# Kernel optimization log

Measured on AMD Instinct MI355X. Metric: run time of the kernel, lower is better.

Reference implementation:

```python
import jax, jax.numpy as jnp
import numpy as np

T, H, E, F, K, FS = 2048, 2048, 64, 512, 8, 512


def setup_inputs() -> dict:
    key = jax.random.key(0)
    ks = jax.random.split(key, 6)
    s = 0.02
    return {
        "hidden_states": jax.random.normal(ks[0], (T, H), jnp.float32),
        # merged gate: E router logits + 1 shared-expert gate logit
        "W_gate": jax.random.normal(ks[1], (H, E + 1), jnp.float32) * s,
        # per-expert merged gate_up proj: [E, H, 2F]
        "W_gate_up": jax.random.normal(ks[2], (E, H, 2 * F), jnp.float32) * s,
        "W_down": jax.random.normal(ks[3], (E, F, H), jnp.float32) * s,
        # shared expert
        "Ws_gate_up": jax.random.normal(ks[4], (H, 2 * FS), jnp.float32) * s,
        "Ws_down": jax.random.normal(ks[5], (FS, H), jnp.float32) * s,
    }


def reference(hidden_states, W_gate, W_gate_up, W_down, Ws_gate_up, Ws_down):
    x = hidden_states  # [T, H]
    logits_all = x @ W_gate                      # [T, E+1]
    router_logits = logits_all[:, :E]
    shared_gate_logit = logits_all[:, E:]        # [T, 1]

    # FusedMoE routing: softmax -> top_k -> renormalize (norm_topk_prob=True)
    probs = jax.nn.softmax(router_logits.astype(jnp.float32), axis=-1)
    topk_w, topk_idx = jax.lax.top_k(probs, K)   # [T, K]
    topk_w = topk_w / jnp.sum(topk_w, axis=-1, keepdims=True)
    # dense combine weights [T, E] (zero for unselected experts)
    combine = jnp.zeros((T, E), probs.dtype).at[
        jnp.arange(T)[:, None], topk_idx].set(topk_w)

    # grouped expert GEMMs (dense reference: every expert sees all tokens,
    # combine-weights zero-out unrouted pairs)
    gu = jnp.einsum('th,ehf->etf', x, W_gate_up)   # [E, T, 2F]
    g, u = jnp.split(gu, 2, axis=-1)
    act = jax.nn.silu(g) * u                       # [E, T, F]
    # apply combine weight before down-proj to avoid [E, T, H] intermediate
    act = act * combine.T[:, :, None].astype(act.dtype)
    routed = jnp.einsum('etf,efh->th', act, W_down)  # [T, H]

    # shared expert (Qwen3NextMLP with sigmoid expert_gate)
    sgu = x @ Ws_gate_up                           # [T, 2FS]
    sg, su = jnp.split(sgu, 2, axis=-1)
    shared = (jax.nn.silu(sg) * su) @ Ws_down      # [T, H]
    shared = jax.nn.sigmoid(shared_gate_logit) * shared

    return shared + routed.astype(x.dtype)
```

## Files before the change

kernel.cpp:

```cpp
#include <hip/hip_runtime.h>
#include <hip/hip_bf16.h>
#include <math.h>

#define T_TOK 2048
#define H_DIM 2048
#define E_NUM 64
#define F_DIM 512
#define K_TOP 8
#define FS_DIM 512
#define NROWS (T_TOK * K_TOP)

typedef __attribute__((ext_vector_type(8))) short short8v;
typedef __attribute__((ext_vector_type(4))) float f32x4;

static __device__ __forceinline__ unsigned short f2bf(float f) {
    unsigned int u = __float_as_uint(f);
    u += 0x7fff + ((u >> 16) & 1);
    return (unsigned short)(u >> 16);
}

__global__ __launch_bounds__(256) void cvt_bf16_kernel(
    const float* __restrict__ in, unsigned short* __restrict__ out, int n8)
{
    int i = blockIdx.x * 256 + threadIdx.x;
    if (i < n8) {
        const float4* p = (const float4*)(in + (size_t)i * 8);
        float4 v0 = p[0], v1 = p[1];
        ushort4 a = make_ushort4(f2bf(v0.x), f2bf(v0.y), f2bf(v0.z), f2bf(v0.w));
        ushort4 b = make_ushort4(f2bf(v1.x), f2bf(v1.y), f2bf(v1.z), f2bf(v1.w));
        ushort4* q = (ushort4*)(out + (size_t)i * 8);
        q[0] = a; q[1] = b;
    }
}

__global__ __launch_bounds__(64) void router_kernel(
    const float* __restrict__ x, const float* __restrict__ Wg,
    int* __restrict__ topk_idx, float* __restrict__ topk_w,
    float* __restrict__ sgate, int* __restrict__ counts)
{
    const int t = blockIdx.x;
    const int lane = threadIdx.x;
    const float* xr = x + (size_t)t * H_DIM;

    float a0 = 0.f, a1 = 0.f, a2 = 0.f, a3 = 0.f;
    for (int h = 0; h < H_DIM; h += 4) {
        float4 xv = *(const float4*)&xr[h];
        a0 += xv.x * Wg[(h + 0) * 65 + lane];
        a1 += xv.y * Wg[(h + 1) * 65 + lane];
        a2 += xv.z * Wg[(h + 2) * 65 + lane];
        a3 += xv.w * Wg[(h + 3) * 65 + lane];
    }
    float logit = (a0 + a1) + (a2 + a3);

    float a64 = 0.f;
    for (int h = lane; h < H_DIM; h += 64) a64 += xr[h] * Wg[h * 65 + 64];
#pragma unroll
    for (int off = 32; off >= 1; off >>= 1) a64 += __shfl_xor(a64, off);

    float v = logit;
    float selv[K_TOP]; int seli[K_TOP];
#pragma unroll
    for (int k = 0; k < K_TOP; ++k) {
        float mv = v; int mi = lane;
#pragma unroll
        for (int off = 32; off >= 1; off >>= 1) {
            float ov = __shfl_xor(mv, off);
            int   oi = __shfl_xor(mi, off);
            if (ov > mv || (ov == mv && oi < mi)) { mv = ov; mi = oi; }
        }
        selv[k] = mv; seli[k] = mi;
        if (lane == mi) v = -INFINITY;
    }

    if (lane == 0) {
        float m = selv[0];
        float w[K_TOP]; float s = 0.f;
#pragma unroll
        for (int k = 0; k < K_TOP; ++k) { w[k] = __expf(selv[k] - m); s += w[k]; }
        float inv = 1.f / s;
#pragma unroll
        for (int k = 0; k < K_TOP; ++k) {
            topk_idx[t * K_TOP + k] = seli[k];
            topk_w[t * K_TOP + k] = w[k] * inv;
            atomicAdd(&counts[seli[k]], 1);
        }
        sgate[t] = 1.f / (1.f + __expf(-a64));
    }
}

__global__ __launch_bounds__(256) void bucket_kernel(
    const int* __restrict__ topk_idx, const float* __restrict__ topk_w,
    const int* __restrict__ counts, int* __restrict__ offsets,
    int* __restrict__ bucket_tok, float* __restrict__ bucket_w)
{
    const int e = blockIdx.x, thr = threadIdx.x;
    __shared__ int cnt[256];
    __shared__ int base_s;
    const int q0 = thr * 64;
    int c = 0;
    for (int q = 0; q < 64; ++q) c += (topk_idx[q0 + q] == e) ? 1 : 0;
    cnt[thr] = c;
    __syncthreads();
    if (thr == 0) {
        int off = 0;
        for (int i = 0; i < e; ++i) off += counts[i];
        offsets[e] = off;
        base_s = off;
        int run = 0;
        for (int i = 0; i < 256; ++i) { int tval = cnt[i]; cnt[i] = run; run += tval; }
    }
    __syncthreads();
    int pos = base_s + cnt[thr];
    for (int q = 0; q < 64; ++q) {
        int pp = q0 + q;
        if (topk_idx[pp] == e) {
            bucket_tok[pos] = pp >> 3;
            bucket_w[pos] = topk_w[pp];
            ++pos;
        }
    }
}

template<int FM, bool ROUTED>
__global__ __launch_bounds__(512, 4) void gu_mfma_kernel(
    const unsigned short* __restrict__ xb,
    const float* __restrict__ Wall,
    const int* __restrict__ counts, const int* __restrict__ offsets,
    const int* __restrict__ bucket_tok, const float* __restrict__ bucket_w,
    unsigned short* __restrict__ actout)
{
    constexpr int BM = FM * 64;
    __shared__ __align__(16) unsigned short Bs[64 * 64];
    __shared__ int   toksS[BM];
    __shared__ float twsS[BM];

    const int tid  = threadIdx.x;
    const int lane = tid & 63;
    const int wid  = tid >> 6;
    const int wm = wid >> 1, wn = wid & 1;
    const int lrow = lane & 15, lhi = lane >> 4;
    const int lr7  = lrow & 7;

    const int c0 = blockIdx.x * 32;
    int ne, base;
    const float* W;
    if (ROUTED) {
        int e = blockIdx.y;
        ne = counts[e]; base = offsets[e];
        W = Wall + (size_t)e * H_DIM * (2 * F_DIM);
    } else {
        ne = T_TOK; base = 0;
        W = Wall;
    }

    const int n4 = (tid & 15) * 4;
    const int kb = (tid >> 4) * 2;
    const int n5 = n4 & 31;
    const int wcol = ((n5 < 16) ? 0 : (F_DIM - 16)) + c0 + (n4 >> 5) * 16 + n5;

    const int m0_beg = ROUTED ? 0 : blockIdx.y * BM;
    const int m0_end = ROUTED ? ne : m0_beg + BM;

    for (int m0 = m0_beg; m0 < m0_end; m0 += BM) {
        __syncthreads();
        for (int i = tid; i < BM; i += 512) {
            if (ROUTED) {
                int idx = m0 + i; bool v = idx < ne;
                toksS[i] = v ? bucket_tok[base + idx] : bucket_tok[base];
                twsS[i]  = v ? bucket_w[base + idx] : 0.f;
            } else {
                toksS[i] = m0 + i; twsS[i] = 1.f;
            }
        }
        __syncthreads();

        const unsigned short* aptr[FM];
#pragma unroll
        for (int fm = 0; fm < FM; ++fm) {
            int r = wm * (FM * 16) + fm * 16 + lrow;
            aptr[fm] = xb + (size_t)toksS[r] * H_DIM;
        }

        f32x4 acc[FM][2];
#pragma unroll
        for (int i = 0; i < FM; ++i) {
            acc[i][0] = (f32x4){0.f, 0.f, 0.f, 0.f};
            acc[i][1] = (f32x4){0.f, 0.f, 0.f, 0.f};
        }

        float4 b0 = *(const float4*)&W[(size_t)kb * (2 * F_DIM) + wcol];
        float4 b1 = *(const float4*)&W[(size_t)(kb + 1) * (2 * F_DIM) + wcol];

        const int NT = H_DIM / 64;
        for (int kt = 0; kt < NT; ++kt) {
#pragma unroll
            for (int cc = 0; cc < 4; ++cc) {
                int n = n4 + cc;
                int idx = n * 64 + ((((kb >> 3) ^ (n & 7)) << 3)) + (kb & 7);
                ushort2 p = make_ushort2(f2bf(((const float*)&b0)[cc]),
                                         f2bf(((const float*)&b1)[cc]));
                *(ushort2*)&Bs[idx] = p;
            }
            __syncthreads();
            if (kt + 1 < NT) {
                const int k0n = (kt + 1) * 64;
                b0 = *(const float4*)&W[(size_t)(k0n + kb) * (2 * F_DIM) + wcol];
                b1 = *(const float4*)&W[(size_t)(k0n + kb + 1) * (2 * F_DIM) + wcol];
            }
            const int k0 = kt * 64;
#pragma unroll
            for (int ks = 0; ks < 2; ++ks) {
                const int kc = ks * 4 + lhi;
                short8v bg = *(const short8v*)&Bs[(wn * 32 + lrow) * 64 + ((kc ^ lr7) << 3)];
                short8v bu = *(const short8v*)&Bs[(wn * 32 + 16 + lrow) * 64 + ((kc ^ lr7) << 3)];
                const int koff = k0 + kc * 8;
#pragma unroll
                for (int fm = 0; fm < FM; ++fm) {
                    short8v af = *(const short8v*)(aptr[fm] + koff);
                    acc[fm][0] = __builtin_amdgcn_mfma_f32_16x16x32_bf16(af, bg, acc[fm][0], 0, 0, 0);
                    acc[fm][1] = __builtin_amdgcn_mfma_f32_16x16x32_bf16(af, bu, acc[fm][1], 0, 0, 0);
                }
            }
            __syncthreads();
        }

        const int acol = c0 + wn * 16 + lrow;
#pragma unroll
        for (int fm = 0; fm < FM; ++fm) {
#pragma unroll
            for (int i = 0; i < 4; ++i) {
                int ml = wm * (FM * 16) + fm * 16 + lhi * 4 + i;
                int idx = m0 + ml;
                if (!ROUTED || idx < ne) {
                    float gv = acc[fm][0][i], uv = acc[fm][1][i];
                    float s = gv / (1.f + __expf(-gv));
                    float val = s * uv * twsS[ml];
                    size_t orow = ROUTED ? (size_t)(base + idx) : (size_t)idx;
                    actout[orow * F_DIM + acol] = f2bf(val);
                }
            }
        }
    }
}

template<int FM, bool ROUTED>
__global__ __launch_bounds__(512, 4) void down_mfma_kernel(
    const unsigned short* __restrict__ actb,
    const float* __restrict__ Wall,
    const int* __restrict__ counts, const int* __restrict__ offsets,
    const int* __restrict__ bucket_tok, const float* __restrict__ sgate,
    float* __restrict__ out)
{
    constexpr int BM = FM * 64;
    __shared__ __align__(16) unsigned short Bs[64 * 64];
    __shared__ int   toksS[BM];
    __shared__ float sgS[BM];

    const int tid  = threadIdx.x;
    const int lane = tid & 63;
    const int wid  = tid >> 6;
    const int wm = wid >> 1, wn = wid & 1;
    const int lrow = lane & 15, lhi = lane >> 4;
    const int lr7  = lrow & 7;

    const int c0 = blockIdx.x * 64;
    int ne, base;
    const float* W;
    if (ROUTED) {
        int e = blockIdx.y;
        ne = counts[e]; base = offsets[e];
        W = Wall + (size_t)e * F_DIM * H_DIM;
    } else {
        ne = T_TOK; base = 0;
        W = Wall;
    }

    const int n4 = (tid & 15) * 4;
    const int kb = (tid >> 4) * 2;
    const int wcol = c0 + n4;

    const int m0_beg = ROUTED ? 0 : blockIdx.y * BM;
    const int m0_end = ROUTED ? ne : m0_beg + BM;

    for (int m0 = m0_beg; m0 < m0_end; m0 += BM) {
        __syncthreads();
        for (int i = tid; i < BM; i += 512) {
            if (ROUTED) {
                int idx = m0 + i;
                toksS[i] = (idx < ne) ? bucket_tok[base + idx] : 0;
            } else {
                sgS[i] = sgate[m0 + i];
            }
        }
        __syncthreads();

        const unsigned short* aptr[FM];
#pragma unroll
        for (int fm = 0; fm < FM; ++fm) {
            int r = wm * (FM * 16) + fm * 16 + lrow;
            int grow = ROUTED ? min(base + m0 + r, NROWS - 1) : (m0 + r);
            aptr[fm] = actb + (size_t)grow * F_DIM;
        }

        f32x4 acc[FM][2];
#pragma unroll
        for (int i = 0; i < FM; ++i) {
            acc[i][0] = (f32x4){0.f, 0.f, 0.f, 0.f};
            acc[i][1] = (f32x4){0.f, 0.f, 0.f, 0.f};
        }

        float4 b0 = *(const float4*)&W[(size_t)kb * H_DIM + wcol];
        float4 b1 = *(const float4*)&W[(size_t)(kb + 1) * H_DIM + wcol];

        const int NT = F_DIM / 64;
        for (int kt = 0; kt < NT; ++kt) {
#pragma unroll
            for (int cc = 0; cc < 4; ++cc) {
                int n = n4 + cc;
                int idx = n * 64 + ((((kb >> 3) ^ (n & 7)) << 3)) + (kb & 7);
                ushort2 p = make_ushort2(f2bf(((const float*)&b0)[cc]),
                                         f2bf(((const float*)&b1)[cc]));
                *(ushort2*)&Bs[idx] = p;
            }
            __syncthreads();
            if (kt + 1 < NT) {
                const int k0n = (kt + 1) * 64;
                b0 = *(const float4*)&W[(size_t)(k0n + kb) * H_DIM + wcol];
                b1 = *(const float4*)&W[(size_t)(k0n + kb + 1) * H_DIM + wcol];
            }
            const int k0 = kt * 64;
#pragma unroll
            for (int ks = 0; ks < 2; ++ks) {
                const int kc = ks * 4 + lhi;
                short8v bf0 = *(const short8v*)&Bs[(wn * 32 + lrow) * 64 + ((kc ^ lr7) << 3)];
                short8v bf1 = *(const short8v*)&Bs[(wn * 32 + 16 + lrow) * 64 + ((kc ^ lr7) << 3)];
                const int koff = k0 + kc * 8;
#pragma unroll
                for (int fm = 0; fm < FM; ++fm) {
                    short8v af = *(const short8v*)(aptr[fm] + koff);
                    acc[fm][0] = __builtin_amdgcn_mfma_f32_16x16x32_bf16(af, bf0, acc[fm][0], 0, 0, 0);
                    acc[fm][1] = __builtin_amdgcn_mfma_f32_16x16x32_bf16(af, bf1, acc[fm][1], 0, 0, 0);
                }
            }
            __syncthreads();
        }

#pragma unroll
        for (int fm = 0; fm < FM; ++fm) {
#pragma unroll
            for (int fn = 0; fn < 2; ++fn) {
                int col = c0 + wn * 32 + fn * 16 + lrow;
#pragma unroll
                for (int i = 0; i < 4; ++i) {
                    int ml = wm * (FM * 16) + fm * 16 + lhi * 4 + i;
                    int idx = m0 + ml;
                    if (ROUTED) {
                        if (idx < ne)
                            atomicAdd(&out[(size_t)toksS[ml] * H_DIM + col], acc[fm][fn][i]);
                    } else {
                        out[(size_t)idx * H_DIM + col] = sgS[ml] * acc[fm][fn][i];
                    }
                }
            }
        }
    }
}

extern "C" void kernel_launch(void* const* d_in, const int* in_sizes, int n_in,
                              void* d_out, int out_size, void* d_ws, size_t ws_size,
                              hipStream_t stream) {
    const float* x    = (const float*)d_in[0];
    const float* Wg   = (const float*)d_in[1];
    const float* Wgu  = (const float*)d_in[2];
    const float* Wd   = (const float*)d_in[3];
    const float* Wsgu = (const float*)d_in[4];
    const float* Wsd  = (const float*)d_in[5];
    float* out = (float*)d_out;

    char* p = (char*)d_ws;
    auto alloc = [&](size_t bytes) {
        char* r = p;
        p += (bytes + 255) & ~(size_t)255;
        return r;
    };
    int*   topk_idx   = (int*)  alloc((size_t)T_TOK * K_TOP * sizeof(int));
    float* topk_w     = (float*)alloc((size_t)T_TOK * K_TOP * sizeof(float));
    float* sgate      = (float*)alloc((size_t)T_TOK * sizeof(float));
    int*   counts     = (int*)  alloc((size_t)E_NUM * sizeof(int));
    int*   offsets    = (int*)  alloc((size_t)E_NUM * sizeof(int));
    int*   bucket_tok = (int*)  alloc((size_t)NROWS * sizeof(int));
    float* bucket_w   = (float*)alloc((size_t)NROWS * sizeof(float));
    unsigned short* xb    = (unsigned short*)alloc((size_t)T_TOK * H_DIM * sizeof(short));
    unsigned short* act_r = (unsigned short*)alloc((size_t)NROWS * F_DIM * sizeof(short));
    unsigned short* act_s = (unsigned short*)alloc((size_t)T_TOK * FS_DIM * sizeof(short));

    hipMemsetAsync(counts, 0, E_NUM * sizeof(int), stream);
    cvt_bf16_kernel<<<(T_TOK * H_DIM / 8 + 255) / 256, 256, 0, stream>>>(x, xb, T_TOK * H_DIM / 8);
    router_kernel<<<T_TOK, 64, 0, stream>>>(x, Wg, topk_idx, topk_w, sgate, counts);
    bucket_kernel<<<E_NUM, 256, 0, stream>>>(topk_idx, topk_w, counts, offsets, bucket_tok, bucket_w);

    gu_mfma_kernel<5, true><<<dim3(16, E_NUM), 512, 0, stream>>>(
        xb, Wgu, counts, offsets, bucket_tok, bucket_w, act_r);
    gu_mfma_kernel<2, false><<<dim3(16, T_TOK / 128), 512, 0, stream>>>(
        xb, Wsgu, counts, offsets, bucket_tok, bucket_w, act_s);

    down_mfma_kernel<2, false><<<dim3(32, T_TOK / 128), 512, 0, stream>>>(
        act_s, Wsd, counts, offsets, bucket_tok, sgate, out);
    down_mfma_kernel<5, true><<<dim3(32, E_NUM), 512, 0, stream>>>(
        act_r, Wd, counts, offsets, bucket_tok, sgate, out);
}
```

Measured before the change: 866.0 us.

## Double-buffer weight tiles in LDS, prefetch A fragments, remap routed blocks across XCDs

Both MFMA GEMM kernels now keep two LDS buffers for the bf16 weight tile, so the next tile is converted and stored while the current one is consumed. That cuts one barrier per k-step. A-operand fragments for the whole k-tile are loaded into registers before the MFMAs. The XOR swizzle is replaced with a padded row stride of 72. Routed launches become 1D grids whose block index is permuted so that blocks of the same expert land on the same XCD, aiming at better L2 reuse of expert weights. The cost is doubled LDS and more registers per thread, which may reduce occupancy under launch_bounds(512,4).

```diff
diff --git a/kernel.cpp b/kernel.cpp
--- a/kernel.cpp
+++ b/kernel.cpp
@@ -130,7 +130,8 @@
     unsigned short* __restrict__ actout)
 {
     constexpr int BM = FM * 64;
-    __shared__ __align__(16) unsigned short Bs[64 * 64];
+    constexpr int BST = 72;
+    __shared__ __align__(16) unsigned short Bs[2][64 * BST];
     __shared__ int   toksS[BM];
     __shared__ float twsS[BM];
 
@@ -139,19 +140,20 @@
     const int wid  = tid >> 6;
     const int wm = wid >> 1, wn = wid & 1;
     const int lrow = lane & 15, lhi = lane >> 4;
-    const int lr7  = lrow & 7;
-
-    const int c0 = blockIdx.x * 32;
-    int ne, base;
+
+    int cblk, ne, base;
     const float* W;
     if (ROUTED) {
-        int e = blockIdx.y;
+        int nw = (blockIdx.x & 7) * ((int)gridDim.x >> 3) + (blockIdx.x >> 3);
+        int e = nw >> 4; cblk = nw & 15;
         ne = counts[e]; base = offsets[e];
         W = Wall + (size_t)e * H_DIM * (2 * F_DIM);
     } else {
+        cblk = blockIdx.x;
         ne = T_TOK; base = 0;
         W = Wall;
     }
+    const int c0 = cblk * 32;
 
     const int n4 = (tid & 15) * 4;
     const int kb = (tid >> 4) * 2;
@@ -188,37 +190,55 @@
             acc[i][1] = (f32x4){0.f, 0.f, 0.f, 0.f};
         }
 
-        float4 b0 = *(const float4*)&W[(size_t)kb * (2 * F_DIM) + wcol];
-        float4 b1 = *(const float4*)&W[(size_t)(kb + 1) * (2 * F_DIM) + wcol];
+        {
+            float4 b0 = *(const float4*)&W[(size_t)kb * (2 * F_DIM) + wcol];
+            float4 b1 = *(const float4*)&W[(size_t)(kb + 1) * (2 * F_DIM) + wcol];
+#pragma unroll
+            for (int cc = 0; cc < 4; ++cc) {
+                ushort2 pk = make_ushort2(f2bf(((const float*)&b0)[cc]),
+                                          f2bf(((const float*)&b1)[cc]));
+                *(ushort2*)&Bs[0][(n4 + cc) * BST + kb] = pk;
+            }
+        }
+        __syncthreads();
 
         const int NT = H_DIM / 64;
         for (int kt = 0; kt < NT; ++kt) {
-#pragma unroll
-            for (int cc = 0; cc < 4; ++cc) {
-                int n = n4 + cc;
-                int idx = n * 64 + ((((kb >> 3) ^ (n & 7)) << 3)) + (kb & 7);
-                ushort2 p = make_ushort2(f2bf(((const float*)&b0)[cc]),
-                                         f2bf(((const float*)&b1)[cc]));
-                *(ushort2*)&Bs[idx] = p;
-            }
-            __syncthreads();
+            const int k0 = kt * 64;
+            const unsigned short* curB = Bs[kt & 1];
+            unsigned short* nxtB = Bs[(kt & 1) ^ 1];
+
+            short8v a[2][FM];
+#pragma unroll
+            for (int ks = 0; ks < 2; ++ks)
+#pragma unroll
+                for (int fm = 0; fm < FM; ++fm)
+                    a[ks][fm] = *(const short8v*)(aptr[fm] + k0 + (ks * 4 + lhi) * 8);
+
+            float4 b0, b1;
             if (kt + 1 < NT) {
-                const int k0n = (kt + 1) * 64;
-                b0 = *(const float4*)&W[(size_t)(k0n + kb) * (2 * F_DIM) + wcol];
-                b1 = *(const float4*)&W[(size_t)(k0n + kb + 1) * (2 * F_DIM) + wcol];
-            }
-            const int k0 = kt * 64;
+                b0 = *(const float4*)&W[(size_t)(k0 + 64 + kb) * (2 * F_DIM) + wcol];
+                b1 = *(const float4*)&W[(size_t)(k0 + 64 + kb + 1) * (2 * F_DIM) + wcol];
+            }
+
 #pragma unroll
             for (int ks = 0; ks < 2; ++ks) {
                 const int kc = ks * 4 + lhi;
-                short8v bg = *(const short8v*)&Bs[(wn * 32 + lrow) * 64 + ((kc ^ lr7) << 3)];
-                short8v bu = *(const short8v*)&Bs[(wn * 32 + 16 + lrow) * 64 + ((kc ^ lr7) << 3)];
-                const int koff = k0 + kc * 8;
+                short8v bg = *(const short8v*)&curB[(wn * 32 + lrow) * BST + kc * 8];
+                short8v bu = *(const short8v*)&curB[(wn * 32 + 16 + lrow) * BST + kc * 8];
 #pragma unroll
                 for (int fm = 0; fm < FM; ++fm) {
-                    short8v af = *(const short8v*)(aptr[fm] + koff);
-                    acc[fm][0] = __builtin_amdgcn_mfma_f32_16x16x32_bf16(af, bg, acc[fm][0], 0, 0, 0);
-                    acc[fm][1] = __builtin_amdgcn_mfma_f32_16x16x32_bf16(af, bu, acc[fm][1], 0, 0, 0);
+                    acc[fm][0] = __builtin_amdgcn_mfma_f32_16x16x32_bf16(a[ks][fm], bg, acc[fm][0], 0, 0, 0);
+                    acc[fm][1] = __builtin_amdgcn_mfma_f32_16x16x32_bf16(a[ks][fm], bu, acc[fm][1], 0, 0, 0);
+                }
+            }
+
+            if (kt + 1 < NT) {
+#pragma unroll
+                for (int cc = 0; cc < 4; ++cc) {
+                    ushort2 pk = make_ushort2(f2bf(((const float*)&b0)[cc]),
+                                              f2bf(((const float*)&b1)[cc]));
+                    *(ushort2*)&nxtB[(n4 + cc) * BST + kb] = pk;
                 }
             }
             __syncthreads();
@@ -252,7 +272,8 @@
     float* __restrict__ out)
 {
     constexpr int BM = FM * 64;
-    __shared__ __align__(16) unsigned short Bs[64 * 64];
+    constexpr int BST = 72;
+    __shared__ __align__(16) unsigned short Bs[2][64 * BST];
     __shared__ int   toksS[BM];
     __shared__ float sgS[BM];
 
@@ -261,19 +282,20 @@
     const int wid  = tid >> 6;
     const int wm = wid >> 1, wn = wid & 1;
     const int lrow = lane & 15, lhi = lane >> 4;
-    const int lr7  = lrow & 7;
-
-    const int c0 = blockIdx.x * 64;
-    int ne, base;
+
+    int cblk, ne, base;
     const float* W;
     if (ROUTED) {
-        int e = blockIdx.y;
+        int nw = (blockIdx.x & 7) * ((int)gridDim.x >> 3) + (blockIdx.x >> 3);
+        int e = nw >> 5; cblk = nw & 31;
         ne = counts[e]; base = offsets[e];
         W = Wall + (size_t)e * F_DIM * H_DIM;
     } else {
+        cblk = blockIdx.x;
         ne = T_TOK; base = 0;
         W = Wall;
     }
+    const int c0 = cblk * 64;
 
     const int n4 = (tid & 15) * 4;
     const int kb = (tid >> 4) * 2;
@@ -309,37 +331,55 @@
             acc[i][1] = (f32x4){0.f, 0.f, 0.f, 0.f};
         }
 
-        float4 b0 = *(const float4*)&W[(size_t)kb * H_DIM + wcol];
-        float4 b1 = *(const float4*)&W[(size_t)(kb + 1) * H_DIM + wcol];
+        {
+            float4 b0 = *(const float4*)&W[(size_t)kb * H_DIM + wcol];
+            float4 b1 = *(const float4*)&W[(size_t)(kb + 1) * H_DIM + wcol];
+#pragma unroll
+            for (int cc = 0; cc < 4; ++cc) {
+                ushort2 pk = make_ushort2(f2bf(((const float*)&b0)[cc]),
+                                          f2bf(((const float*)&b1)[cc]));
+                *(ushort2*)&Bs[0][(n4 + cc) * BST + kb] = pk;
+            }
+        }
+        __syncthreads();
 
         const int NT = F_DIM / 64;
         for (int kt = 0; kt < NT; ++kt) {
-#pragma unroll
-            for (int cc = 0; cc < 4; ++cc) {
-                int n = n4 + cc;
-                int idx = n * 64 + ((((kb >> 3) ^ (n & 7)) << 3)) + (kb & 7);
-                ushort2 p = make_ushort2(f2bf(((const float*)&b0)[cc]),
-                                         f2bf(((const float*)&b1)[cc]));
-                *(ushort2*)&Bs[idx] = p;
-            }
-            __syncthreads();
+            const int k0 = kt * 64;
+            const unsigned short* curB = Bs[kt & 1];
+            unsigned short* nxtB = Bs[(kt & 1) ^ 1];
+
+            short8v a[2][FM];
+#pragma unroll
+            for (int ks = 0; ks < 2; ++ks)
+#pragma unroll
+                for (int fm = 0; fm < FM; ++fm)
+                    a[ks][fm] = *(const short8v*)(aptr[fm] + k0 + (ks * 4 + lhi) * 8);
+
+            float4 b0, b1;
             if (kt + 1 < NT) {
-                const int k0n = (kt + 1) * 64;
-                b0 = *(const float4*)&W[(size_t)(k0n + kb) * H_DIM + wcol];
-                b1 = *(const float4*)&W[(size_t)(k0n + kb + 1) * H_DIM + wcol];
-            }
-            const int k0 = kt * 64;
+                b0 = *(const float4*)&W[(size_t)(k0 + 64 + kb) * H_DIM + wcol];
+                b1 = *(const float4*)&W[(size_t)(k0 + 64 + kb + 1) * H_DIM + wcol];
+            }
+
 #pragma unroll
             for (int ks = 0; ks < 2; ++ks) {
                 const int kc = ks * 4 + lhi;
-                short8v bf0 = *(const short8v*)&Bs[(wn * 32 + lrow) * 64 + ((kc ^ lr7) << 3)];
-                short8v bf1 = *(const short8v*)&Bs[(wn * 32 + 16 + lrow) * 64 + ((kc ^ lr7) << 3)];
-                const int koff = k0 + kc * 8;
+                short8v bf0 = *(const short8v*)&curB[(wn * 32 + lrow) * BST + kc * 8];
+                short8v bf1 = *(const short8v*)&curB[(wn * 32 + 16 + lrow) * BST + kc * 8];
 #pragma unroll
                 for (int fm = 0; fm < FM; ++fm) {
-                    short8v af = *(const short8v*)(aptr[fm] + koff);
-                    acc[fm][0] = __builtin_amdgcn_mfma_f32_16x16x32_bf16(af, bf0, acc[fm][0], 0, 0, 0);
-                    acc[fm][1] = __builtin_amdgcn_mfma_f32_16x16x32_bf16(af, bf1, acc[fm][1], 0, 0, 0);
+                    acc[fm][0] = __builtin_amdgcn_mfma_f32_16x16x32_bf16(a[ks][fm], bf0, acc[fm][0], 0, 0, 0);
+                    acc[fm][1] = __builtin_amdgcn_mfma_f32_16x16x32_bf16(a[ks][fm], bf1, acc[fm][1], 0, 0, 0);
+                }
+            }
+
+            if (kt + 1 < NT) {
+#pragma unroll
+                for (int cc = 0; cc < 4; ++cc) {
+                    ushort2 pk = make_ushort2(f2bf(((const float*)&b0)[cc]),
+                                              f2bf(((const float*)&b1)[cc]));
+                    *(ushort2*)&nxtB[(n4 + cc) * BST + kb] = pk;
                 }
             }
             __syncthreads();
@@ -399,13 +439,13 @@
     router_kernel<<<T_TOK, 64, 0, stream>>>(x, Wg, topk_idx, topk_w, sgate, counts);
     bucket_kernel<<<E_NUM, 256, 0, stream>>>(topk_idx, topk_w, counts, offsets, bucket_tok, bucket_w);
 
-    gu_mfma_kernel<5, true><<<dim3(16, E_NUM), 512, 0, stream>>>(
+    gu_mfma_kernel<5, true><<<16 * E_NUM, 512, 0, stream>>>(
         xb, Wgu, counts, offsets, bucket_tok, bucket_w, act_r);
     gu_mfma_kernel<2, false><<<dim3(16, T_TOK / 128), 512, 0, stream>>>(
         xb, Wsgu, counts, offsets, bucket_tok, bucket_w, act_s);
 
     down_mfma_kernel<2, false><<<dim3(32, T_TOK / 128), 512, 0, stream>>>(
         act_s, Wsd, counts, offsets, bucket_tok, sgate, out);
-    down_mfma_kernel<5, true><<<dim3(32, E_NUM), 512, 0, stream>>>(
+    down_mfma_kernel<5, true><<<32 * E_NUM, 512, 0, stream>>>(
         act_r, Wd, counts, offsets, bucket_tok, sgate, out);
 }
```

After: 817.7 us. 1.06x faster.

## Stage activation tiles in LDS via direct global-to-LDS loads and split expert M-tiles

Applied to the files above, without the earlier changes.

Both grouped GEMM kernels now stage the A (token/activation) tile into swizzled shared memory with global_load_lds, instead of having each wave read it straight from global memory. The M tile grows to 256 rows and each expert's rows are split across two M-tile blocks striding by 512, with a remapped 1D grid so experts spread across XCDs. Blocks with no rows exit early. This targets redundant global A reads and poor load balance across experts. In exchange it uses more LDS per block, asks for higher occupancy through launch bounds, and pads tail rows with clamped indices.

```diff
diff --git a/kernel.cpp b/kernel.cpp
--- a/kernel.cpp
+++ b/kernel.cpp
@@ -18,6 +18,14 @@
     u += 0x7fff + ((u >> 16) & 1);
     return (unsigned short)(u >> 16);
 }
+
+#define BCHUNK(row, k8) ((((k8) ^ ((row) + ((row) >> 3)))) & 7)
+#define ASWZ(row) (((row) + ((row) >> 3)) & 7)
+
+typedef const unsigned int __attribute__((address_space(1))) gu32;
+typedef unsigned int __attribute__((address_space(3))) lu32;
+#define GLDS16(gsrc, ldst) \
+    __builtin_amdgcn_global_load_lds((gu32*)(gsrc), (lu32*)(ldst), 16, 0, 0)
 
 __global__ __launch_bounds__(256) void cvt_bf16_kernel(
     const float* __restrict__ in, unsigned short* __restrict__ out, int n8)
@@ -121,15 +129,16 @@
     }
 }
 
-template<int FM, bool ROUTED>
-__global__ __launch_bounds__(512, 4) void gu_mfma_kernel(
+template<bool ROUTED>
+__global__ __launch_bounds__(512, 6) void gu_mfma_kernel(
     const unsigned short* __restrict__ xb,
     const float* __restrict__ Wall,
     const int* __restrict__ counts, const int* __restrict__ offsets,
     const int* __restrict__ bucket_tok, const float* __restrict__ bucket_w,
     unsigned short* __restrict__ actout)
 {
-    constexpr int BM = FM * 64;
+    constexpr int BM = 256;
+    __shared__ __align__(16) unsigned short As[BM * 64];
     __shared__ __align__(16) unsigned short Bs[64 * 64];
     __shared__ int   toksS[BM];
     __shared__ float twsS[BM];
@@ -139,99 +148,121 @@
     const int wid  = tid >> 6;
     const int wm = wid >> 1, wn = wid & 1;
     const int lrow = lane & 15, lhi = lane >> 4;
-    const int lr7  = lrow & 7;
-
-    const int c0 = blockIdx.x * 32;
-    int ne, base;
+
+    int cblk, mt, ne, base;
     const float* W;
     if (ROUTED) {
-        int e = blockIdx.y;
+        int nw = (blockIdx.x & 7) * ((int)gridDim.x >> 3) + (blockIdx.x >> 3);
+        int e = nw >> 5; mt = (nw >> 4) & 1; cblk = nw & 15;
         ne = counts[e]; base = offsets[e];
+        if (mt * BM >= ne) return;
         W = Wall + (size_t)e * H_DIM * (2 * F_DIM);
     } else {
+        cblk = blockIdx.x; mt = blockIdx.y;
         ne = T_TOK; base = 0;
         W = Wall;
     }
+    const int c0 = cblk * 32;
 
     const int n4 = (tid & 15) * 4;
     const int kb = (tid >> 4) * 2;
     const int n5 = n4 & 31;
     const int wcol = ((n5 < 16) ? 0 : (F_DIM - 16)) + c0 + (n4 >> 5) * 16 + n5;
-
-    const int m0_beg = ROUTED ? 0 : blockIdx.y * BM;
-    const int m0_end = ROUTED ? ne : m0_beg + BM;
-
-    for (int m0 = m0_beg; m0 < m0_end; m0 += BM) {
+    int wr_off[4];
+#pragma unroll
+    for (int cc = 0; cc < 4; ++cc) {
+        int n = n4 + cc;
+        wr_off[cc] = n * 64 + BCHUNK(n, kb >> 3) * 8 + (kb & 7);
+    }
+    const int rg = wn * 32 + lrow, ru = wn * 32 + 16 + lrow;
+    int rdBg[2], rdBu[2];
+#pragma unroll
+    for (int ks = 0; ks < 2; ++ks) {
+        int kc = ks * 4 + lhi;
+        rdBg[ks] = rg * 64 + BCHUNK(rg, kc) * 8;
+        rdBu[ks] = ru * 64 + BCHUNK(ru, kc) * 8;
+    }
+    int rdA[4][2];
+#pragma unroll
+    for (int fm = 0; fm < 4; ++fm) {
+        int arow = wm * 64 + fm * 16 + lrow;
+#pragma unroll
+        for (int ks = 0; ks < 2; ++ks) {
+            int kc = ks * 4 + lhi;
+            rdA[fm][ks] = arow * 64 + (((kc ^ ASWZ(arow)) & 7) << 3);
+        }
+    }
+    const int m0_stride = ROUTED ? (2 * BM) : ((int)gridDim.y * BM);
+
+    for (int m0 = mt * BM; m0 < ne; m0 += m0_stride) {
         __syncthreads();
-        for (int i = tid; i < BM; i += 512) {
+        if (tid < BM) {
+            int idx = m0 + tid; bool v = idx < ne;
             if (ROUTED) {
-                int idx = m0 + i; bool v = idx < ne;
-                toksS[i] = v ? bucket_tok[base + idx] : bucket_tok[base];
-                twsS[i]  = v ? bucket_w[base + idx] : 0.f;
+                toksS[tid] = v ? bucket_tok[base + idx] : bucket_tok[base];
+                twsS[tid]  = v ? bucket_w[base + idx] : 0.f;
             } else {
-                toksS[i] = m0 + i; twsS[i] = 1.f;
+                toksS[tid] = v ? idx : (T_TOK - 1);
+                twsS[tid]  = 1.f;
             }
         }
         __syncthreads();
 
-        const unsigned short* aptr[FM];
-#pragma unroll
-        for (int fm = 0; fm < FM; ++fm) {
-            int r = wm * (FM * 16) + fm * 16 + lrow;
-            aptr[fm] = xb + (size_t)toksS[r] * H_DIM;
-        }
-
-        f32x4 acc[FM][2];
-#pragma unroll
-        for (int i = 0; i < FM; ++i) {
+        int asrc[4];
+#pragma unroll
+        for (int i = 0; i < 4; ++i) {
+            int row = wid * 32 + i * 8 + (lane >> 3);
+            asrc[i] = toksS[row] * H_DIM + (((lane & 7) ^ ASWZ(row)) << 3);
+        }
+
+        f32x4 acc[4][2];
+#pragma unroll
+        for (int i = 0; i < 4; ++i) {
             acc[i][0] = (f32x4){0.f, 0.f, 0.f, 0.f};
             acc[i][1] = (f32x4){0.f, 0.f, 0.f, 0.f};
         }
 
+        const int NT = H_DIM / 64;
         float4 b0 = *(const float4*)&W[(size_t)kb * (2 * F_DIM) + wcol];
         float4 b1 = *(const float4*)&W[(size_t)(kb + 1) * (2 * F_DIM) + wcol];
 
-        const int NT = H_DIM / 64;
         for (int kt = 0; kt < NT; ++kt) {
-#pragma unroll
-            for (int cc = 0; cc < 4; ++cc) {
-                int n = n4 + cc;
-                int idx = n * 64 + ((((kb >> 3) ^ (n & 7)) << 3)) + (kb & 7);
-                ushort2 p = make_ushort2(f2bf(((const float*)&b0)[cc]),
-                                         f2bf(((const float*)&b1)[cc]));
-                *(ushort2*)&Bs[idx] = p;
-            }
+            const int k0 = kt * 64;
             __syncthreads();
-            if (kt + 1 < NT) {
-                const int k0n = (kt + 1) * 64;
-                b0 = *(const float4*)&W[(size_t)(k0n + kb) * (2 * F_DIM) + wcol];
-                b1 = *(const float4*)&W[(size_t)(k0n + kb + 1) * (2 * F_DIM) + wcol];
-            }
-            const int k0 = kt * 64;
+#pragma unroll
+            for (int i = 0; i < 4; ++i)
+                GLDS16(xb + asrc[i] + k0, &As[(wid * 32 + i * 8) * 64]);
+#pragma unroll
+            for (int cc = 0; cc < 4; ++cc)
+                *(ushort2*)&Bs[wr_off[cc]] = make_ushort2(
+                    f2bf(((const float*)&b0)[cc]), f2bf(((const float*)&b1)[cc]));
+            {
+                int knx = (kt + 1 < NT) ? (k0 + 64) : k0;
+                b0 = *(const float4*)&W[(size_t)(knx + kb) * (2 * F_DIM) + wcol];
+                b1 = *(const float4*)&W[(size_t)(knx + kb + 1) * (2 * F_DIM) + wcol];
+            }
+            __syncthreads();
 #pragma unroll
             for (int ks = 0; ks < 2; ++ks) {
-                const int kc = ks * 4 + lhi;
-                short8v bg = *(const short8v*)&Bs[(wn * 32 + lrow) * 64 + ((kc ^ lr7) << 3)];
-                short8v bu = *(const short8v*)&Bs[(wn * 32 + 16 + lrow) * 64 + ((kc ^ lr7) << 3)];
-                const int koff = k0 + kc * 8;
-#pragma unroll
-                for (int fm = 0; fm < FM; ++fm) {
-                    short8v af = *(const short8v*)(aptr[fm] + koff);
+                short8v bg = *(const short8v*)&Bs[rdBg[ks]];
+                short8v bu = *(const short8v*)&Bs[rdBu[ks]];
+#pragma unroll
+                for (int fm = 0; fm < 4; ++fm) {
+                    short8v af = *(const short8v*)&As[rdA[fm][ks]];
                     acc[fm][0] = __builtin_amdgcn_mfma_f32_16x16x32_bf16(af, bg, acc[fm][0], 0, 0, 0);
                     acc[fm][1] = __builtin_amdgcn_mfma_f32_16x16x32_bf16(af, bu, acc[fm][1], 0, 0, 0);
                 }
             }
-            __syncthreads();
         }
 
         const int acol = c0 + wn * 16 + lrow;
 #pragma unroll
-        for (int fm = 0; fm < FM; ++fm) {
+        for (int fm = 0; fm < 4; ++fm) {
 #pragma unroll
             for (int i = 0; i < 4; ++i) {
-                int ml = wm * (FM * 16) + fm * 16 + lhi * 4 + i;
+                int ml = wm * 64 + fm * 16 + lhi * 4 + i;
                 int idx = m0 + ml;
-                if (!ROUTED || idx < ne) {
+                if (idx < ne) {
                     float gv = acc[fm][0][i], uv = acc[fm][1][i];
                     float s = gv / (1.f + __expf(-gv));
                     float val = s * uv * twsS[ml];
@@ -243,15 +274,16 @@
     }
 }
 
-template<int FM, bool ROUTED>
-__global__ __launch_bounds__(512, 4) void down_mfma_kernel(
+template<bool ROUTED>
+__global__ __launch_bounds__(512, 6) void down_mfma_kernel(
     const unsigned short* __restrict__ actb,
     const float* __restrict__ Wall,
     const int* __restrict__ counts, const int* __restrict__ offsets,
     const int* __restrict__ bucket_tok, const float* __restrict__ sgate,
     float* __restrict__ out)
 {
-    constexpr int BM = FM * 64;
+    constexpr int BM = 256;
+    __shared__ __align__(16) unsigned short As[BM * 64];
     __shared__ __align__(16) unsigned short Bs[64 * 64];
     __shared__ int   toksS[BM];
     __shared__ float sgS[BM];
@@ -261,104 +293,127 @@
     const int wid  = tid >> 6;
     const int wm = wid >> 1, wn = wid & 1;
     const int lrow = lane & 15, lhi = lane >> 4;
-    const int lr7  = lrow & 7;
-
-    const int c0 = blockIdx.x * 64;
-    int ne, base;
+
+    int cblk, mt, ne, base;
     const float* W;
     if (ROUTED) {
-        int e = blockIdx.y;
+        int nw = (blockIdx.x & 7) * ((int)gridDim.x >> 3) + (blockIdx.x >> 3);
+        int e = nw >> 6; mt = (nw >> 5) & 1; cblk = nw & 31;
         ne = counts[e]; base = offsets[e];
+        if (mt * BM >= ne) return;
         W = Wall + (size_t)e * F_DIM * H_DIM;
     } else {
+        cblk = blockIdx.x; mt = blockIdx.y;
         ne = T_TOK; base = 0;
         W = Wall;
     }
+    const int c0 = cblk * 64;
 
     const int n4 = (tid & 15) * 4;
     const int kb = (tid >> 4) * 2;
     const int wcol = c0 + n4;
-
-    const int m0_beg = ROUTED ? 0 : blockIdx.y * BM;
-    const int m0_end = ROUTED ? ne : m0_beg + BM;
-
-    for (int m0 = m0_beg; m0 < m0_end; m0 += BM) {
+    int wr_off[4];
+#pragma unroll
+    for (int cc = 0; cc < 4; ++cc) {
+        int n = n4 + cc;
+        wr_off[cc] = n * 64 + BCHUNK(n, kb >> 3) * 8 + (kb & 7);
+    }
+    const int r0 = wn * 32 + lrow, r1 = wn * 32 + 16 + lrow;
+    int rdB0[2], rdB1[2];
+#pragma unroll
+    for (int ks = 0; ks < 2; ++ks) {
+        int kc = ks * 4 + lhi;
+        rdB0[ks] = r0 * 64 + BCHUNK(r0, kc) * 8;
+        rdB1[ks] = r1 * 64 + BCHUNK(r1, kc) * 8;
+    }
+    int rdA[4][2];
+#pragma unroll
+    for (int fm = 0; fm < 4; ++fm) {
+        int arow = wm * 64 + fm * 16 + lrow;
+#pragma unroll
+        for (int ks = 0; ks < 2; ++ks) {
+            int kc = ks * 4 + lhi;
+            rdA[fm][ks] = arow * 64 + (((kc ^ ASWZ(arow)) & 7) << 3);
+        }
+    }
+    const int m0_stride = ROUTED ? (2 * BM) : ((int)gridDim.y * BM);
+
+    for (int m0 = mt * BM; m0 < ne; m0 += m0_stride) {
         __syncthreads();
-        for (int i = tid; i < BM; i += 512) {
+        if (tid < BM) {
+            int idx = m0 + tid;
             if (ROUTED) {
-                int idx = m0 + i;
-                toksS[i] = (idx < ne) ? bucket_tok[base + idx] : 0;
+                toksS[tid] = (idx < ne) ? bucket_tok[base + idx] : 0;
             } else {
-                sgS[i] = sgate[m0 + i];
+                sgS[tid] = sgate[(idx < ne) ? idx : (T_TOK - 1)];
             }
         }
         __syncthreads();
 
-        const unsigned short* aptr[FM];
-#pragma unroll
-        for (int fm = 0; fm < FM; ++fm) {
-            int r = wm * (FM * 16) + fm * 16 + lrow;
-            int grow = ROUTED ? min(base + m0 + r, NROWS - 1) : (m0 + r);
-            aptr[fm] = actb + (size_t)grow * F_DIM;
-        }
-
-        f32x4 acc[FM][2];
-#pragma unroll
-        for (int i = 0; i < FM; ++i) {
+        int asrc[4];
+#pragma unroll
+        for (int i = 0; i < 4; ++i) {
+            int row = wid * 32 + i * 8 + (lane >> 3);
+            int grow = ROUTED ? min(base + m0 + row, NROWS - 1)
+                              : min(m0 + row, T_TOK - 1);
+            asrc[i] = grow * F_DIM + (((lane & 7) ^ ASWZ(row)) << 3);
+        }
+
+        f32x4 acc[4][2];
+#pragma unroll
+        for (int i = 0; i < 4; ++i) {
             acc[i][0] = (f32x4){0.f, 0.f, 0.f, 0.f};
             acc[i][1] = (f32x4){0.f, 0.f, 0.f, 0.f};
         }
 
+        const int NT = F_DIM / 64;
         float4 b0 = *(const float4*)&W[(size_t)kb * H_DIM + wcol];
         float4 b1 = *(const float4*)&W[(size_t)(kb + 1) * H_DIM + wcol];
 
-        const int NT = F_DIM / 64;
         for (int kt = 0; kt < NT; ++kt) {
-#pragma unroll
-            for (int cc = 0; cc < 4; ++cc) {
-                int n = n4 + cc;
-                int idx = n * 64 + ((((kb >> 3) ^ (n & 7)) << 3)) + (kb & 7);
-                ushort2 p = make_ushort2(f2bf(((const float*)&b0)[cc]),
-                                         f2bf(((const float*)&b1)[cc]));
-                *(ushort2*)&Bs[idx] = p;
-            }
+            const int k0 = kt * 64;
             __syncthreads();
-            if (kt + 1 < NT) {
-                const int k0n = (kt + 1) * 64;
-                b0 = *(const float4*)&W[(size_t)(k0n + kb) * H_DIM + wcol];
-                b1 = *(const float4*)&W[(size_t)(k0n + kb + 1) * H_DIM + wcol];
-            }
-            const int k0 = kt * 64;
+#pragma unroll
+            for (int i = 0; i < 4; ++i)
+                GLDS16(actb + asrc[i] + k0, &As[(wid * 32 + i * 8) * 64]);
+#pragma unroll
+            for (int cc = 0; cc < 4; ++cc)
+                *(ushort2*)&Bs[wr_off[cc]] = make_ushort2(
+                    f2bf(((const float*)&b0)[cc]), f2bf(((const float*)&b1)[cc]));
+            {
+                int knx = (kt + 1 < NT) ? (k0 + 64) : k0;
+                b0 = *(const float4*)&W[(size_t)(knx + kb) * H_DIM + wcol];
+                b1 = *(const float4*)&W[(size_t)(knx + kb + 1) * H_DIM + wcol];
+            }
+            __syncthreads();
 #pragma unroll
             for (int ks = 0; ks < 2; ++ks) {
-                const int kc = ks * 4 + lhi;
-                short8v bf0 = *(const short8v*)&Bs[(wn * 32 + lrow) * 64 + ((kc ^ lr7) << 3)];
-                short8v bf1 = *(const short8v*)&Bs[(wn * 32 + 16 + lrow) * 64 + ((kc ^ lr7) << 3)];
-                const int koff = k0 + kc * 8;
-#pragma unroll
-                for (int fm = 0; fm < FM; ++fm) {
-                    short8v af = *(const short8v*)(aptr[fm] + koff);
+                short8v bf0 = *(const short8v*)&Bs[rdB0[ks]];
+                short8v bf1 = *(const short8v*)&Bs[rdB1[ks]];
+#pragma unroll
+                for (int fm = 0; fm < 4; ++fm) {
+                    short8v af = *(const short8v*)&As[rdA[fm][ks]];
                     acc[fm][0] = __builtin_amdgcn_mfma_f32_16x16x32_bf16(af, bf0, acc[fm][0], 0, 0, 0);
                     acc[fm][1] = __builtin_amdgcn_mfma_f32_16x16x32_bf16(af, bf1, acc[fm][1], 0, 0, 0);
                 }
             }
-            __syncthreads();
-        }
-
-#pragma unroll
-        for (int fm = 0; fm < FM; ++fm) {
+        }
+
+#pragma unroll
+        for (int fm = 0; fm < 4; ++fm) {
 #pragma unroll
             for (int fn = 0; fn < 2; ++fn) {
                 int col = c0 + wn * 32 + fn * 16 + lrow;
 #pragma unroll
                 for (int i = 0; i < 4; ++i) {
-                    int ml = wm * (FM * 16) + fm * 16 + lhi * 4 + i;
+                    int ml = wm * 64 + fm * 16 + lhi * 4 + i;
                     int idx = m0 + ml;
-                    if (ROUTED) {
-                        if (idx < ne)
+                    if (idx < ne) {
+                        if (ROUTED) {
                             atomicAdd(&out[(size_t)toksS[ml] * H_DIM + col], acc[fm][fn][i]);
-                    } else {
-                        out[(size_t)idx * H_DIM + col] = sgS[ml] * acc[fm][fn][i];
+                        } else {
+                            out[(size_t)idx * H_DIM + col] = sgS[ml] * acc[fm][fn][i];
+                        }
                     }
                 }
             }
@@ -399,13 +454,13 @@
     router_kernel<<<T_TOK, 64, 0, stream>>>(x, Wg, topk_idx, topk_w, sgate, counts);
     bucket_kernel<<<E_NUM, 256, 0, stream>>>(topk_idx, topk_w, counts, offsets, bucket_tok, bucket_w);
 
-    gu_mfma_kernel<5, true><<<dim3(16, E_NUM), 512, 0, stream>>>(
+    gu_mfma_kernel<true><<<16 * E_NUM * 2, 512, 0, stream>>>(
         xb, Wgu, counts, offsets, bucket_tok, bucket_w, act_r);
-    gu_mfma_kernel<2, false><<<dim3(16, T_TOK / 128), 512, 0, stream>>>(
+    gu_mfma_kernel<false><<<dim3(16, T_TOK / 256), 512, 0, stream>>>(
         xb, Wsgu, counts, offsets, bucket_tok, bucket_w, act_s);
 
-    down_mfma_kernel<2, false><<<dim3(32, T_TOK / 128), 512, 0, stream>>>(
+    down_mfma_kernel<false><<<dim3(32, T_TOK / 256), 512, 0, stream>>>(
         act_s, Wsd, counts, offsets, bucket_tok, sgate, out);
-    down_mfma_kernel<5, true><<<dim3(32, E_NUM), 512, 0, stream>>>(
+    down_mfma_kernel<true><<<32 * E_NUM * 2, 512, 0, stream>>>(
         act_r, Wd, counts, offsets, bucket_tok, sgate, out);
 }
```

Result: faster. 819.7 us (-5.3%).
